# Performance work log

Hardware: AMD Instinct MI355X
Metric: run time of the kernel (lower is better)

## Reference

```python
import jax, jax.numpy as jnp
import numpy as np
from jax import lax

B, CIN, IMG, K = 128, 3, 112, 7
C = 1024      # hidden_channels * channel_dilation
HID = 512     # hidden_channels
HW = (IMG // K) ** 2  # 256 patches
EPS = 1e-5


def _prelu(x, a):
    return jnp.where(x > 0, x, a * x)


def _bn(x, g, b):
    # BatchNorm2d with track_running_stats=False: always uses batch stats
    m = x.mean(axis=(0, 2, 3), keepdims=True)
    v = x.var(axis=(0, 2, 3), keepdims=True)
    return (x - m) * lax.rsqrt(v + EPS) * g[None, :, None, None] + b[None, :, None, None]


def setup_inputs() -> dict:
    key = jax.random.key(0)
    ks = jax.random.split(key, 16)
    d = {
        'x':  jax.random.normal(ks[0], (B, CIN, IMG, IMG), jnp.float32),
        'w0': jax.random.normal(ks[1], (C, CIN, K, K), jnp.float32) * 0.05,
        'b0': jax.random.normal(ks[2], (C,), jnp.float32) * 0.01,
        'a0': jnp.full((1,), 0.25, jnp.float32),
    }
    for i in range(1, 4):
        kw, kb = jax.random.split(jax.random.fold_in(key, i))
        d[f'w{i}'] = jax.random.normal(kw, (C, C), jnp.float32) * 0.02
        d[f'b{i}'] = jax.random.normal(kb, (C,), jnp.float32) * 0.01
        d[f'g{i}'] = jnp.ones((C,), jnp.float32)
        d[f'bt{i}'] = jnp.zeros((C,), jnp.float32)
        d[f'p{i}'] = jnp.full((1,), 0.25, jnp.float32)
    d['pos'] = jax.random.normal(ks[3], (1, HW, C), jnp.float32)
    d['am'] = jnp.full((1,), 0.25, jnp.float32)
    d['wm'] = jax.random.normal(ks[4], (HID, C), jnp.float32) * 0.03
    d['bm'] = jax.random.normal(ks[5], (HID,), jnp.float32) * 0.01
    pkeys = jax.random.split(ks[6], B)
    d['perm'] = jax.vmap(lambda k: jax.random.permutation(k, HW))(pkeys).astype(jnp.int32)
    return d


def reference(x, w0, b0, a0,
              w1, b1, g1, bt1, p1,
              w2, b2, g2, bt2, p2,
              w3, b3, g3, bt3, p3,
              pos, am, wm, bm, perm):
    # patch-embed conv: stride = kernel_size -> [B, C, 16, 16]
    h = lax.conv_general_dilated(x, w0, (K, K), 'VALID',
                                 dimension_numbers=('NCHW', 'OIHW', 'NCHW'))
    h = _prelu(h + b0[None, :, None, None], a0)
    for w, b, g, bt, p in ((w1, b1, g1, bt1, p1),
                           (w2, b2, g2, bt2, p2),
                           (w3, b3, g3, bt3, p3)):
        h = jnp.einsum('bchw,dc->bdhw', h, w) + b[None, :, None, None]  # 1x1 conv
        h = _prelu(_bn(h, g, bt), p)
    Bn, Cn, Hn, Wn = h.shape
    enc = h.reshape(Bn, Cn, Hn * Wn).transpose(0, 2, 1)  # [B, HW, C]
    enc = enc + pos                                      # private: add pos embedding
    enc = _prelu(enc, am) @ wm.T + bm                    # mixer -> [B, HW, HID]
    # private: per-sample token permutation (single batched gather)
    return jnp.take_along_axis(enc, perm[:, :, None], axis=1)
```

## Files before the change

kernel.cpp:

```cpp
#include <hip/hip_runtime.h>
#include <hip/hip_bf16.h>
#include <stdint.h>


typedef __attribute__((ext_vector_type(8))) short bf16x8;
typedef __attribute__((ext_vector_type(4))) float f32x4;

__device__ __forceinline__ float bf2f(uint32_t u) {
  union { uint32_t i; float f; } v; v.i = u << 16; return v.f;
}
__device__ __forceinline__ ushort f2bf(float f) {
  union { float f; uint32_t i; } v; v.f = f;
  uint32_t i = v.i;
  return (ushort)((i + 0x7FFFu + ((i >> 16) & 1u)) >> 16);
}

template<int EPI, int XB>
__global__ void __launch_bounds__(512, 2)
gemm_kernel(const ushort* __restrict__ A, const ushort* __restrict__ Bw,
            const float* __restrict__ bias, const float* __restrict__ alpha,
            void* __restrict__ outp, float* __restrict__ part,
            const int* __restrict__ inv, int K, int Dout)
{
  __shared__ __align__(16) ushort At[2][256 * 64];
  __shared__ __align__(16) ushort Bt[2][256 * 64];
  const int tid  = threadIdx.x;
  const int lane = tid & 63;
  const int wid  = tid >> 6;
  const int wm   = wid >> 2;
  const int wn   = wid & 3;

  const int s = blockIdx.x;
  const int j = s >> 3;
  const int x = j & ((1 << XB) - 1);
  const int y = ((j >> XB) << 3) | (s & 7);
  const int t0 = y << 8;
  const int d0 = x << 8;

  f32x4 acc[8][4] = {};

  const int lrow8 = lane >> 3;
  const int csrc  = (lane & 7) ^ lrow8;
  const int NT = K >> 6;

  auto stage = [&](int t, int buf) {
    const int k0 = t << 6;
#pragma unroll
    for (int g = 0; g < 4; ++g) {
      int rb = (g << 6) + (wid << 3);
      const ushort* ga = A + (size_t)(t0 + rb + lrow8) * K + k0 + (csrc << 3);
      __builtin_amdgcn_global_load_lds(
          (const __attribute__((address_space(1))) uint32_t*)ga,
          (__attribute__((address_space(3))) uint32_t*)(&At[buf][rb << 6]), 16, 0, 0);
      const ushort* gb = Bw + (size_t)(d0 + rb + lrow8) * K + k0 + (csrc << 3);
      __builtin_amdgcn_global_load_lds(
          (const __attribute__((address_space(1))) uint32_t*)gb,
          (__attribute__((address_space(3))) uint32_t*)(&Bt[buf][rb << 6]), 16, 0, 0);
    }
  };

  stage(0, 0);
  stage(1, 1);

  for (int t = 0; t < NT; ++t) {
    const int cur = t & 1;
    if (t + 1 < NT) { asm volatile("s_waitcnt vmcnt(8)" ::: "memory"); }
    else            { asm volatile("s_waitcnt vmcnt(0)" ::: "memory"); }
    __builtin_amdgcn_s_barrier();

    __builtin_amdgcn_s_setprio(1);
#pragma unroll
    for (int kk = 0; kk < 2; ++kk) {
      const int kc = (kk << 2) + (lane >> 4);
      bf16x8 af[8], bfr[4];
#pragma unroll
      for (int m = 0; m < 8; ++m) {
        int row = (wm << 7) + (m << 4) + (lane & 15);
        af[m] = *(const bf16x8*)&At[cur][(row << 6) + ((kc ^ (row & 7)) << 3)];
      }
#pragma unroll
      for (int n = 0; n < 4; ++n) {
        int col = (wn << 6) + (n << 4) + (lane & 15);
        bfr[n] = *(const bf16x8*)&Bt[cur][(col << 6) + ((kc ^ (col & 7)) << 3)];
      }
#pragma unroll
      for (int m = 0; m < 8; ++m)
#pragma unroll
        for (int n = 0; n < 4; ++n)
          acc[m][n] = __builtin_amdgcn_mfma_f32_16x16x32_bf16(af[m], bfr[n], acc[m][n], 0, 0, 0);
    }
    __builtin_amdgcn_s_setprio(0);
    asm volatile("s_waitcnt lgkmcnt(0)" ::: "memory");
    __builtin_amdgcn_s_barrier();
    asm volatile("" ::: "memory");
    if (t + 2 < NT) stage(t + 2, cur);
  }

  float a0v = (EPI == 0) ? alpha[0] : 0.0f;
  float sA[4], s2A[4];
#pragma unroll
  for (int n = 0; n < 4; ++n) { sA[n] = 0.f; s2A[n] = 0.f; }

#pragma unroll
  for (int n = 0; n < 4; ++n) {
    int d = d0 + (wn << 6) + (n << 4) + (lane & 15);
    float bs = bias[d];
#pragma unroll
    for (int m = 0; m < 8; ++m) {
      int tb = t0 + (wm << 7) + (m << 4) + ((lane >> 4) << 2);
#pragma unroll
      for (int r = 0; r < 4; ++r) {
        float v = acc[m][n][r] + bs;
        if (EPI == 0) v = v > 0.f ? v : a0v * v;
        if (EPI == 1) { sA[n] += v; s2A[n] += v * v; }
        if (EPI == 2) {
          int row = tb + r;
          int orow = (row & ~255) | inv[row];
          ((float*)outp)[(size_t)orow * Dout + d] = v;
        } else {
          ((ushort*)outp)[(size_t)(tb + r) * Dout + d] = f2bf(v);
        }
      }
    }
  }

  if (EPI == 1) {
    float2* sm = (float2*)&At[0][0];
    int slot = (wm << 2) | (lane >> 4);
#pragma unroll
    for (int n = 0; n < 4; ++n) {
      int c = (wn << 6) + (n << 4) + (lane & 15);
      sm[slot * 256 + c] = make_float2(sA[n], s2A[n]);
    }
    __syncthreads();
    if (tid < 256) {
      float ss = 0.f, ss2 = 0.f;
      for (int q = 0; q < 8; ++q) {
        float2 v = sm[q * 256 + tid];
        ss += v.x; ss2 += v.y;
      }
      part[(size_t)y * 2048 + d0 + tid]        = ss;
      part[(size_t)y * 2048 + 1024 + d0 + tid] = ss2;
    }
  }
}

__global__ void bnfold_kernel(const float* __restrict__ part, const float* __restrict__ g,
                              const float* __restrict__ bt, float* __restrict__ scsh) {
  int d = (blockIdx.x << 8) + threadIdx.x;
  float s = 0.f, s2 = 0.f;
  for (int j = 0; j < 128; ++j) { s += part[j * 2048 + d]; s2 += part[j * 2048 + 1024 + d]; }
  float mean = s * (1.f / 32768.f);
  float var  = s2 * (1.f / 32768.f) - mean * mean;
  float sc = g[d] * rsqrtf(var + 1e-5f);
  scsh[d] = sc;
  scsh[1024 + d] = bt[d] - mean * sc;
}

template<bool MIX>
__global__ void bnact_kernel(ushort* __restrict__ Y, const float* __restrict__ scsh,
                             const float* __restrict__ p, const float* __restrict__ pos,
                             const float* __restrict__ am) {
  size_t i = (((size_t)blockIdx.x << 8) + threadIdx.x) << 3;
  int d = (int)(i & 1023);
  float pp = p[0];
  float aa = MIX ? am[0] : 0.f;
  float pv[8];
  if (MIX) {
    int prow = (int)((i >> 10) & 255);
    const float4* pb = (const float4*)(pos + ((size_t)prow << 10) + d);
    float4 pA = pb[0], pB = pb[1];
    pv[0]=pA.x; pv[1]=pA.y; pv[2]=pA.z; pv[3]=pA.w;
    pv[4]=pB.x; pv[5]=pB.y; pv[6]=pB.z; pv[7]=pB.w;
  }
  uint4 raw = *(const uint4*)(Y + i);
  uint32_t w[4] = {raw.x, raw.y, raw.z, raw.w};
  uint32_t o[4];
#pragma unroll
  for (int q = 0; q < 4; ++q) {
    int dd = d + q * 2;
    float v0 = bf2f(w[q] & 0xFFFFu) * scsh[dd]     + scsh[1024 + dd];
    float v1 = bf2f(w[q] >> 16)     * scsh[dd + 1] + scsh[1024 + dd + 1];
    v0 = v0 > 0.f ? v0 : pp * v0;
    v1 = v1 > 0.f ? v1 : pp * v1;
    if (MIX) {
      v0 += pv[2 * q];     v1 += pv[2 * q + 1];
      v0 = v0 > 0.f ? v0 : aa * v0;
      v1 = v1 > 0.f ? v1 : aa * v1;
    }
    o[q] = (uint32_t)f2bf(v0) | ((uint32_t)f2bf(v1) << 16);
  }
  *(uint4*)(Y + i) = make_uint4(o[0], o[1], o[2], o[3]);
}

__global__ void invperm_kernel(const int* __restrict__ perm, int* __restrict__ inv) {
  int t = (blockIdx.x << 8) + threadIdx.x;
  inv[(t & ~255) + perm[t]] = t & 255;
}

__global__ void f2b_kernel(const float* __restrict__ in, ushort* __restrict__ out, int n) {
  int i = (blockIdx.x << 8) + threadIdx.x;
  if (i < n) out[i] = f2bf(in[i]);
}

__global__ void padw0_kernel(const float* __restrict__ w0, ushort* __restrict__ o) {
  int d = blockIdx.x, j = threadIdx.x;
  o[d * 256 + j] = (j < 147) ? f2bf(w0[d * 147 + j]) : (ushort)0;
}

__global__ void im2col_kernel(const float* __restrict__ x, ushort* __restrict__ P) {
  int t = blockIdx.x;
  int j = threadIdx.x;
  ushort v = 0;
  if (j < 147) {
    int b = t >> 8, pidx = t & 255;
    int pi = pidx >> 4, pj = pidx & 15;
    int cin = j / 49, rem = j - cin * 49;
    int dy = rem / 7, dx = rem - dy * 7;
    v = f2bf(x[(size_t)(b * 3 + cin) * 12544 + (size_t)(pi * 7 + dy) * 112 + (pj * 7 + dx)]);
  }
  P[(size_t)t * 256 + j] = v;
}

extern "C" void kernel_launch(void* const* d_in, const int* in_sizes, int n_in,
                              void* d_out, int out_size, void* d_ws, size_t ws_size,
                              hipStream_t stream) {
  const float* x   = (const float*)d_in[0];
  const float* w0  = (const float*)d_in[1];
  const float* b0  = (const float*)d_in[2];
  const float* a0  = (const float*)d_in[3];
  const float* w1  = (const float*)d_in[4];
  const float* b1  = (const float*)d_in[5];
  const float* g1  = (const float*)d_in[6];
  const float* bt1 = (const float*)d_in[7];
  const float* p1  = (const float*)d_in[8];
  const float* w2  = (const float*)d_in[9];
  const float* b2  = (const float*)d_in[10];
  const float* g2  = (const float*)d_in[11];
  const float* bt2 = (const float*)d_in[12];
  const float* p2  = (const float*)d_in[13];
  const float* w3  = (const float*)d_in[14];
  const float* b3  = (const float*)d_in[15];
  const float* g3  = (const float*)d_in[16];
  const float* bt3 = (const float*)d_in[17];
  const float* p3  = (const float*)d_in[18];
  const float* pos = (const float*)d_in[19];
  const float* am  = (const float*)d_in[20];
  const float* wm  = (const float*)d_in[21];
  const float* bm  = (const float*)d_in[22];
  const int*  perm = (const int*)d_in[23];

  char* ws = (char*)d_ws;
  ushort* B0   = (ushort*)ws;
  ushort* B1   = (ushort*)(ws + 67108864);
  float*  part = (float*)(ws + 134217728);
  float*  scsh = (float*)(ws + 134217728 + 2097152);
  int*    inv  = (int*)  (ws + 134217728 + 2097152 + 8192);
  ushort* wbuf = (ushort*)(ws + 134217728 + 2097152 + 8192 + 131072);

  invperm_kernel<<<dim3(128), dim3(256), 0, stream>>>(perm, inv);
  im2col_kernel<<<dim3(32768), dim3(256), 0, stream>>>(x, B1);
  padw0_kernel<<<dim3(1024), dim3(256), 0, stream>>>(w0, wbuf);

  gemm_kernel<0, 2><<<dim3(512), dim3(512), 0, stream>>>(
      B1, wbuf, b0, a0, (void*)B0, nullptr, nullptr, 256, 1024);

  f2b_kernel<<<dim3(4096), dim3(256), 0, stream>>>(w1, wbuf, 1048576);
  gemm_kernel<1, 2><<<dim3(512), dim3(512), 0, stream>>>(
      B0, wbuf, b1, nullptr, (void*)B1, part, nullptr, 1024, 1024);
  bnfold_kernel<<<dim3(4), dim3(256), 0, stream>>>(part, g1, bt1, scsh);
  bnact_kernel<false><<<dim3(16384), dim3(256), 0, stream>>>(B1, scsh, p1, nullptr, nullptr);

  f2b_kernel<<<dim3(4096), dim3(256), 0, stream>>>(w2, wbuf, 1048576);
  gemm_kernel<1, 2><<<dim3(512), dim3(512), 0, stream>>>(
      B1, wbuf, b2, nullptr, (void*)B0, part, nullptr, 1024, 1024);
  bnfold_kernel<<<dim3(4), dim3(256), 0, stream>>>(part, g2, bt2, scsh);
  bnact_kernel<false><<<dim3(16384), dim3(256), 0, stream>>>(B0, scsh, p2, nullptr, nullptr);

  f2b_kernel<<<dim3(4096), dim3(256), 0, stream>>>(w3, wbuf, 1048576);
  gemm_kernel<1, 2><<<dim3(512), dim3(512), 0, stream>>>(
      B0, wbuf, b3, nullptr, (void*)B1, part, nullptr, 1024, 1024);
  bnfold_kernel<<<dim3(4), dim3(256), 0, stream>>>(part, g3, bt3, scsh);
  bnact_kernel<true><<<dim3(16384), dim3(256), 0, stream>>>(B1, scsh, p3, pos, am);

  f2b_kernel<<<dim3(2048), dim3(256), 0, stream>>>(wm, wbuf, 524288);
  gemm_kernel<2, 1><<<dim3(256), dim3(512), 0, stream>>>(
      B1, wbuf, bm, nullptr, d_out, nullptr, inv, 1024, 512);
}
```

Measured before the change: 468.4 us.

## Interleave LDS reads, global prefetch and MFMA in barrier-separated phases

Restructures the GEMM main loop into four phases per k-tile. Each phase reads a quarter of the A/B fragments from LDS, issues part of the next tile's global-to-LDS loads, and runs 16 MFMAs between barriers, in the style of a ping-pong schedule. A is now prefetched one tile ahead and B two tiles ahead, so memory traffic spreads across the compute. The epilogue hoists the bias loads and computes the gather index once per row. The extra barriers add sync overhead and risk stalls if the waitcnt accounting is off.

Result: faster. 418.4 us (-10.7%).

```diff
diff --git a/kernel.cpp b/kernel.cpp
--- a/kernel.cpp
+++ b/kernel.cpp
@@ -43,83 +43,116 @@
   const int csrc  = (lane & 7) ^ lrow8;
   const int NT = K >> 6;
 
-  auto stage = [&](int t, int buf) {
+  auto stageA = [&](int t, int buf, int h) {
     const int k0 = t << 6;
 #pragma unroll
-    for (int g = 0; g < 4; ++g) {
-      int rb = (g << 6) + (wid << 3);
-      const ushort* ga = A + (size_t)(t0 + rb + lrow8) * K + k0 + (csrc << 3);
+    for (int i = 0; i < 2; ++i) {
+      int rb = (h << 7) + (wid << 4) + (i << 3);
+      const ushort* gp = A + (size_t)(t0 + rb + lrow8) * K + k0 + (csrc << 3);
       __builtin_amdgcn_global_load_lds(
-          (const __attribute__((address_space(1))) uint32_t*)ga,
+          (const __attribute__((address_space(1))) uint32_t*)gp,
           (__attribute__((address_space(3))) uint32_t*)(&At[buf][rb << 6]), 16, 0, 0);
-      const ushort* gb = Bw + (size_t)(d0 + rb + lrow8) * K + k0 + (csrc << 3);
+    }
+  };
+  auto stageB = [&](int t, int buf, int h) {
+    const int k0 = t << 6;
+#pragma unroll
+    for (int i = 0; i < 2; ++i) {
+      int rb = (h << 7) + (wid << 4) + (i << 3);
+      const ushort* gp = Bw + (size_t)(d0 + rb + lrow8) * K + k0 + (csrc << 3);
       __builtin_amdgcn_global_load_lds(
-          (const __attribute__((address_space(1))) uint32_t*)gb,
+          (const __attribute__((address_space(1))) uint32_t*)gp,
           (__attribute__((address_space(3))) uint32_t*)(&Bt[buf][rb << 6]), 16, 0, 0);
     }
   };
-
-  stage(0, 0);
-  stage(1, 1);
+  auto readA = [&](bf16x8* af, int buf, int mh, int kk) {
+    const int kc = (kk << 2) + (lane >> 4);
+#pragma unroll
+    for (int m = 0; m < 4; ++m) {
+      int row = (wm << 7) + (mh << 6) + (m << 4) + (lane & 15);
+      af[m] = *(const bf16x8*)&At[buf][(row << 6) + ((kc ^ (row & 7)) << 3)];
+    }
+  };
+  auto readB = [&](bf16x8* bf, int buf, int kk) {
+    const int kc = (kk << 2) + (lane >> 4);
+#pragma unroll
+    for (int n = 0; n < 4; ++n) {
+      int col = (wn << 6) + (n << 4) + (lane & 15);
+      bf[n] = *(const bf16x8*)&Bt[buf][(col << 6) + ((kc ^ (col & 7)) << 3)];
+    }
+  };
+  auto mfma16 = [&](const bf16x8* af, const bf16x8* bf, int mh) {
+    __builtin_amdgcn_s_setprio(1);
+#pragma unroll
+    for (int m = 0; m < 4; ++m)
+#pragma unroll
+      for (int n = 0; n < 4; ++n)
+        acc[(mh << 2) + m][n] =
+            __builtin_amdgcn_mfma_f32_16x16x32_bf16(af[m], bf[n], acc[(mh << 2) + m][n], 0, 0, 0);
+    __builtin_amdgcn_s_setprio(0);
+  };
+
+  stageA(0, 0, 0); stageA(0, 0, 1);
+  stageB(0, 0, 0); stageB(0, 0, 1);
+  if (NT > 1) { stageB(1, 1, 0); stageB(1, 1, 1); }
+  if (NT > 1) { asm volatile("s_waitcnt vmcnt(4)" ::: "memory"); }
+  else        { asm volatile("s_waitcnt vmcnt(0)" ::: "memory"); }
+  __builtin_amdgcn_s_barrier();
+
+  bf16x8 af[4], bfA[4], bfB[4];
 
   for (int t = 0; t < NT; ++t) {
     const int cur = t & 1;
-    if (t + 1 < NT) { asm volatile("s_waitcnt vmcnt(8)" ::: "memory"); }
-    else            { asm volatile("s_waitcnt vmcnt(0)" ::: "memory"); }
-    __builtin_amdgcn_s_barrier();
-
-    __builtin_amdgcn_s_setprio(1);
-#pragma unroll
-    for (int kk = 0; kk < 2; ++kk) {
-      const int kc = (kk << 2) + (lane >> 4);
-      bf16x8 af[8], bfr[4];
-#pragma unroll
-      for (int m = 0; m < 8; ++m) {
-        int row = (wm << 7) + (m << 4) + (lane & 15);
-        af[m] = *(const bf16x8*)&At[cur][(row << 6) + ((kc ^ (row & 7)) << 3)];
-      }
+    const bool haveN1 = (t + 1 < NT), haveN2 = (t + 2 < NT);
+
+    readA(af, cur, 0, 0);
+    readB(bfA, cur, 0);
+    if (haveN1) stageA(t + 1, cur ^ 1, 0);
+    __builtin_amdgcn_s_barrier();
+    mfma16(af, bfA, 0);
+    __builtin_amdgcn_s_barrier();
+
+    readA(af, cur, 1, 0);
+    if (haveN1) stageA(t + 1, cur ^ 1, 1);
+    __builtin_amdgcn_s_barrier();
+    mfma16(af, bfA, 1);
+    __builtin_amdgcn_s_barrier();
+
+    readA(af, cur, 0, 1);
+    readB(bfB, cur, 1);
+    __builtin_amdgcn_s_barrier();
+    mfma16(af, bfB, 0);
+    __builtin_amdgcn_s_barrier();
+
+    readA(af, cur, 1, 1);
+    if (haveN2) { stageB(t + 2, cur, 0); stageB(t + 2, cur, 1); }
+    if (haveN2)      { asm volatile("s_waitcnt vmcnt(4)" ::: "memory"); }
+    else if (haveN1) { asm volatile("s_waitcnt vmcnt(0)" ::: "memory"); }
+    __builtin_amdgcn_s_barrier();
+    mfma16(af, bfB, 1);
+    __builtin_amdgcn_s_barrier();
+  }
+
+  float bs[4];
+#pragma unroll
+  for (int n = 0; n < 4; ++n) bs[n] = bias[d0 + (wn << 6) + (n << 4) + (lane & 15)];
+  float a0v = (EPI == 0) ? alpha[0] : 0.0f;
+  float sA[4] = {0.f, 0.f, 0.f, 0.f}, s2A[4] = {0.f, 0.f, 0.f, 0.f};
+
+#pragma unroll
+  for (int m = 0; m < 8; ++m) {
+#pragma unroll
+    for (int r = 0; r < 4; ++r) {
+      int row = t0 + (wm << 7) + (m << 4) + ((lane >> 4) << 2) + r;
+      int orow = (EPI == 2) ? ((row & ~255) | inv[row]) : row;
 #pragma unroll
       for (int n = 0; n < 4; ++n) {
-        int col = (wn << 6) + (n << 4) + (lane & 15);
-        bfr[n] = *(const bf16x8*)&Bt[cur][(col << 6) + ((kc ^ (col & 7)) << 3)];
-      }
-#pragma unroll
-      for (int m = 0; m < 8; ++m)
-#pragma unroll
-        for (int n = 0; n < 4; ++n)
-          acc[m][n] = __builtin_amdgcn_mfma_f32_16x16x32_bf16(af[m], bfr[n], acc[m][n], 0, 0, 0);
-    }
-    __builtin_amdgcn_s_setprio(0);
-    asm volatile("s_waitcnt lgkmcnt(0)" ::: "memory");
-    __builtin_amdgcn_s_barrier();
-    asm volatile("" ::: "memory");
-    if (t + 2 < NT) stage(t + 2, cur);
-  }
-
-  float a0v = (EPI == 0) ? alpha[0] : 0.0f;
-  float sA[4], s2A[4];
-#pragma unroll
-  for (int n = 0; n < 4; ++n) { sA[n] = 0.f; s2A[n] = 0.f; }
-
-#pragma unroll
-  for (int n = 0; n < 4; ++n) {
-    int d = d0 + (wn << 6) + (n << 4) + (lane & 15);
-    float bs = bias[d];
-#pragma unroll
-    for (int m = 0; m < 8; ++m) {
-      int tb = t0 + (wm << 7) + (m << 4) + ((lane >> 4) << 2);
-#pragma unroll
-      for (int r = 0; r < 4; ++r) {
-        float v = acc[m][n][r] + bs;
+        int d = d0 + (wn << 6) + (n << 4) + (lane & 15);
+        float v = acc[m][n][r] + bs[n];
         if (EPI == 0) v = v > 0.f ? v : a0v * v;
         if (EPI == 1) { sA[n] += v; s2A[n] += v * v; }
-        if (EPI == 2) {
-          int row = tb + r;
-          int orow = (row & ~255) | inv[row];
-          ((float*)outp)[(size_t)orow * Dout + d] = v;
-        } else {
-          ((ushort*)outp)[(size_t)(tb + r) * Dout + d] = f2bf(v);
-        }
+        if (EPI == 2) ((float*)outp)[(size_t)orow * Dout + d] = v;
+        else          ((ushort*)outp)[(size_t)row * Dout + d] = f2bf(v);
       }
     }
   }
@@ -127,6 +160,7 @@
   if (EPI == 1) {
     float2* sm = (float2*)&At[0][0];
     int slot = (wm << 2) | (lane >> 4);
+    __syncthreads();
 #pragma unroll
     for (int n = 0; n < 4; ++n) {
       int c = (wn << 6) + (n << 4) + (lane & 15);
```

## Restructure GEMM main loop into interleaved half-tile loads and MFMA phases

Applied to the files above, without the earlier changes.

Rewrites the GEMM K-loop as four sub-phases per tile. Each phase issues LDS reads for half the A rows, launches the global-to-LDS copies for the next A tile and for B two tiles ahead, and runs 16 MFMAs between barriers. It also makes K and Dout template constants, precomputes the swizzled LDS addresses, and reorders the epilogue so the inverse-permutation index is loaded once per row. The aim is finer overlap of memory traffic with MFMA work and less address arithmetic, at the cost of many more barriers per tile and a subtler buffer-reuse pattern.

Measured after the change: 405.0 us. 13.5% less time.

```diff
diff --git a/kernel.cpp b/kernel.cpp
--- a/kernel.cpp
+++ b/kernel.cpp
@@ -15,12 +15,12 @@
   return (ushort)((i + 0x7FFFu + ((i >> 16) & 1u)) >> 16);
 }
 
-template<int EPI, int XB>
+template<int EPI, int XB, int K, int DOUT>
 __global__ void __launch_bounds__(512, 2)
 gemm_kernel(const ushort* __restrict__ A, const ushort* __restrict__ Bw,
             const float* __restrict__ bias, const float* __restrict__ alpha,
             void* __restrict__ outp, float* __restrict__ part,
-            const int* __restrict__ inv, int K, int Dout)
+            const int* __restrict__ inv)
 {
   __shared__ __align__(16) ushort At[2][256 * 64];
   __shared__ __align__(16) ushort Bt[2][256 * 64];
@@ -39,87 +39,123 @@
 
   f32x4 acc[8][4] = {};
 
+  const int swz = (((lane >> 4) ^ (lane & 7)) << 4);
+  const char* LA0 = (const char*)&At[0][0] + ((((wm << 7) + (lane & 15))) << 7) + swz;
+  const char* LA1 = (const char*)&At[0][0] + ((((wm << 7) + (lane & 15))) << 7) + (swz ^ 64);
+  const char* LB0 = (const char*)&Bt[0][0] + ((((wn << 6) + (lane & 15))) << 7) + swz;
+  const char* LB1 = (const char*)&Bt[0][0] + ((((wn << 6) + (lane & 15))) << 7) + (swz ^ 64);
+
   const int lrow8 = lane >> 3;
   const int csrc  = (lane & 7) ^ lrow8;
-  const int NT = K >> 6;
-
-  auto stage = [&](int t, int buf) {
-    const int k0 = t << 6;
-#pragma unroll
-    for (int g = 0; g < 4; ++g) {
-      int rb = (g << 6) + (wid << 3);
-      const ushort* ga = A + (size_t)(t0 + rb + lrow8) * K + k0 + (csrc << 3);
-      __builtin_amdgcn_global_load_lds(
-          (const __attribute__((address_space(1))) uint32_t*)ga,
-          (__attribute__((address_space(3))) uint32_t*)(&At[buf][rb << 6]), 16, 0, 0);
-      const ushort* gb = Bw + (size_t)(d0 + rb + lrow8) * K + k0 + (csrc << 3);
-      __builtin_amdgcn_global_load_lds(
-          (const __attribute__((address_space(1))) uint32_t*)gb,
-          (__attribute__((address_space(3))) uint32_t*)(&Bt[buf][rb << 6]), 16, 0, 0);
-    }
-  };
-
-  stage(0, 0);
-  stage(1, 1);
-
-  for (int t = 0; t < NT; ++t) {
-    const int cur = t & 1;
-    if (t + 1 < NT) { asm volatile("s_waitcnt vmcnt(8)" ::: "memory"); }
-    else            { asm volatile("s_waitcnt vmcnt(0)" ::: "memory"); }
-    __builtin_amdgcn_s_barrier();
-
-    __builtin_amdgcn_s_setprio(1);
-#pragma unroll
-    for (int kk = 0; kk < 2; ++kk) {
-      const int kc = (kk << 2) + (lane >> 4);
-      bf16x8 af[8], bfr[4];
-#pragma unroll
-      for (int m = 0; m < 8; ++m) {
-        int row = (wm << 7) + (m << 4) + (lane & 15);
-        af[m] = *(const bf16x8*)&At[cur][(row << 6) + ((kc ^ (row & 7)) << 3)];
-      }
+  const ushort* gAw = A  + (size_t)(t0 + (wid << 4) + lrow8) * K + (csrc << 3);
+  const ushort* gBw = Bw + (size_t)(d0 + (wid << 4) + lrow8) * K + (csrc << 3);
+  char* stA = (char*)&At[0][0] + (wid << 11);
+  char* stB = (char*)&Bt[0][0] + (wid << 11);
+
+#define STAGE_A(T, BUF, H) do {                                                          \
+    __builtin_amdgcn_global_load_lds(                                                    \
+      (const __attribute__((address_space(1))) uint32_t*)(gAw + (size_t)((H)*128)*K + ((size_t)(T) << 6)),     \
+      (__attribute__((address_space(3))) uint32_t*)(stA + (BUF)*32768 + (H)*16384), 16, 0, 0);                  \
+    __builtin_amdgcn_global_load_lds(                                                    \
+      (const __attribute__((address_space(1))) uint32_t*)(gAw + (size_t)((H)*128+8)*K + ((size_t)(T) << 6)),   \
+      (__attribute__((address_space(3))) uint32_t*)(stA + (BUF)*32768 + (H)*16384 + 1024), 16, 0, 0);           \
+  } while (0)
+#define STAGE_B(T, BUF, H) do {                                                          \
+    __builtin_amdgcn_global_load_lds(                                                    \
+      (const __attribute__((address_space(1))) uint32_t*)(gBw + (size_t)((H)*128)*K + ((size_t)(T) << 6)),     \
+      (__attribute__((address_space(3))) uint32_t*)(stB + (BUF)*32768 + (H)*16384), 16, 0, 0);                  \
+    __builtin_amdgcn_global_load_lds(                                                    \
+      (const __attribute__((address_space(1))) uint32_t*)(gBw + (size_t)((H)*128+8)*K + ((size_t)(T) << 6)),   \
+      (__attribute__((address_space(3))) uint32_t*)(stB + (BUF)*32768 + (H)*16384 + 1024), 16, 0, 0);           \
+  } while (0)
+
+#define RD_A(dst, BASE, CUR, MH) do {                                                    \
+    dst[0] = *(const bf16x8*)((BASE) + (CUR)*32768 + (MH)*8192 + 0);                     \
+    dst[1] = *(const bf16x8*)((BASE) + (CUR)*32768 + (MH)*8192 + 2048);                  \
+    dst[2] = *(const bf16x8*)((BASE) + (CUR)*32768 + (MH)*8192 + 4096);                  \
+    dst[3] = *(const bf16x8*)((BASE) + (CUR)*32768 + (MH)*8192 + 6144);                  \
+  } while (0)
+#define RD_B(dst, BASE, CUR) do {                                                        \
+    dst[0] = *(const bf16x8*)((BASE) + (CUR)*32768 + 0);                                 \
+    dst[1] = *(const bf16x8*)((BASE) + (CUR)*32768 + 2048);                              \
+    dst[2] = *(const bf16x8*)((BASE) + (CUR)*32768 + 4096);                              \
+    dst[3] = *(const bf16x8*)((BASE) + (CUR)*32768 + 6144);                              \
+  } while (0)
+#define MFMA16(AF, BF, MH) do {                                                          \
+    __builtin_amdgcn_s_setprio(1);                                                       \
+    _Pragma("unroll")                                                                    \
+    for (int m_ = 0; m_ < 4; ++m_)                                                       \
+      _Pragma("unroll")                                                                  \
+      for (int n_ = 0; n_ < 4; ++n_)                                                     \
+        acc[((MH) << 2) + m_][n_] = __builtin_amdgcn_mfma_f32_16x16x32_bf16(             \
+            AF[m_], BF[n_], acc[((MH) << 2) + m_][n_], 0, 0, 0);                         \
+    __builtin_amdgcn_s_setprio(0);                                                       \
+  } while (0)
+
+#define TILE_BODY(T, CUR, HN1, HN2) do {                                                 \
+    bf16x8 af[4], bfA[4], bfB[4];                                                        \
+                                                                                \
+    RD_A(af, LA0, CUR, 0); RD_B(bfA, LB0, CUR);                                          \
+    if (HN1) STAGE_A((T) + 1, (CUR) ^ 1, 0);                                             \
+    __builtin_amdgcn_s_barrier();                                                        \
+    MFMA16(af, bfA, 0);                                                                  \
+    __builtin_amdgcn_s_barrier();                                                        \
+                                                                                \
+    RD_A(af, LA0, CUR, 1);                                                               \
+    if (HN1) STAGE_A((T) + 1, (CUR) ^ 1, 1);                                             \
+    __builtin_amdgcn_s_barrier();                                                        \
+    MFMA16(af, bfA, 1);                                                                  \
+    __builtin_amdgcn_s_barrier();                                                        \
+                                                                                \
+    RD_A(af, LA1, CUR, 0); RD_B(bfB, LB1, CUR);                                          \
+    __builtin_amdgcn_s_barrier();                                                        \
+    MFMA16(af, bfB, 0);                                                                  \
+    __builtin_amdgcn_s_barrier();                                                        \
+                                                                                \
+    RD_A(af, LA1, CUR, 1);                                                               \
+    if (HN2) { STAGE_B((T) + 2, CUR, 0); STAGE_B((T) + 2, CUR, 1); }                     \
+    if (HN2)      { asm volatile("s_waitcnt vmcnt(4)" ::: "memory"); }                   \
+    else if (HN1) { asm volatile("s_waitcnt vmcnt(0)" ::: "memory"); }                   \
+    __builtin_amdgcn_s_barrier();                                                        \
+    MFMA16(af, bfB, 1);                                                                  \
+    __builtin_amdgcn_s_barrier();                                                        \
+  } while (0)
+
+  constexpr int NT = K >> 6;
+
+  STAGE_A(0, 0, 0); STAGE_A(0, 0, 1);
+  STAGE_B(0, 0, 0); STAGE_B(0, 0, 1);
+  STAGE_B(1, 1, 0); STAGE_B(1, 1, 1);
+  asm volatile("s_waitcnt vmcnt(4)" ::: "memory");
+  __builtin_amdgcn_s_barrier();
+
+#pragma unroll 1
+  for (int tp = 0; tp < NT; tp += 2) {
+    const bool more = (tp + 2 < NT);
+    TILE_BODY(tp,     0, true, more);
+    TILE_BODY(tp + 1, 1, more, more);
+  }
+
+  float bs[4];
+#pragma unroll
+  for (int n = 0; n < 4; ++n) bs[n] = bias[d0 + (wn << 6) + (n << 4) + (lane & 15)];
+  float a0v = (EPI == 0) ? alpha[0] : 0.0f;
+  float sA[4] = {0.f, 0.f, 0.f, 0.f}, s2A[4] = {0.f, 0.f, 0.f, 0.f};
+
+#pragma unroll
+  for (int m = 0; m < 8; ++m) {
+#pragma unroll
+    for (int r = 0; r < 4; ++r) {
+      int row = t0 + (wm << 7) + (m << 4) + ((lane >> 4) << 2) + r;
+      int orow = (EPI == 2) ? ((row & ~255) | inv[row]) : row;
 #pragma unroll
       for (int n = 0; n < 4; ++n) {
-        int col = (wn << 6) + (n << 4) + (lane & 15);
-        bfr[n] = *(const bf16x8*)&Bt[cur][(col << 6) + ((kc ^ (col & 7)) << 3)];
-      }
-#pragma unroll
-      for (int m = 0; m < 8; ++m)
-#pragma unroll
-        for (int n = 0; n < 4; ++n)
-          acc[m][n] = __builtin_amdgcn_mfma_f32_16x16x32_bf16(af[m], bfr[n], acc[m][n], 0, 0, 0);
-    }
-    __builtin_amdgcn_s_setprio(0);
-    asm volatile("s_waitcnt lgkmcnt(0)" ::: "memory");
-    __builtin_amdgcn_s_barrier();
-    asm volatile("" ::: "memory");
-    if (t + 2 < NT) stage(t + 2, cur);
-  }
-
-  float a0v = (EPI == 0) ? alpha[0] : 0.0f;
-  float sA[4], s2A[4];
-#pragma unroll
-  for (int n = 0; n < 4; ++n) { sA[n] = 0.f; s2A[n] = 0.f; }
-
-#pragma unroll
-  for (int n = 0; n < 4; ++n) {
-    int d = d0 + (wn << 6) + (n << 4) + (lane & 15);
-    float bs = bias[d];
-#pragma unroll
-    for (int m = 0; m < 8; ++m) {
-      int tb = t0 + (wm << 7) + (m << 4) + ((lane >> 4) << 2);
-#pragma unroll
-      for (int r = 0; r < 4; ++r) {
-        float v = acc[m][n][r] + bs;
+        int d = d0 + (wn << 6) + (n << 4) + (lane & 15);
+        float v = acc[m][n][r] + bs[n];
         if (EPI == 0) v = v > 0.f ? v : a0v * v;
         if (EPI == 1) { sA[n] += v; s2A[n] += v * v; }
-        if (EPI == 2) {
-          int row = tb + r;
-          int orow = (row & ~255) | inv[row];
-          ((float*)outp)[(size_t)orow * Dout + d] = v;
-        } else {
-          ((ushort*)outp)[(size_t)(tb + r) * Dout + d] = f2bf(v);
-        }
+        if (EPI == 2) ((float*)outp)[(size_t)orow * DOUT + d] = v;
+        else          ((ushort*)outp)[(size_t)row * DOUT + d] = f2bf(v);
       }
     }
   }
@@ -127,6 +163,7 @@
   if (EPI == 1) {
     float2* sm = (float2*)&At[0][0];
     int slot = (wm << 2) | (lane >> 4);
+    __syncthreads();
 #pragma unroll
     for (int n = 0; n < 4; ++n) {
       int c = (wn << 6) + (n << 4) + (lane & 15);
@@ -143,6 +180,12 @@
       part[(size_t)y * 2048 + 1024 + d0 + tid] = ss2;
     }
   }
+#undef STAGE_A
+#undef STAGE_B
+#undef RD_A
+#undef RD_B
+#undef MFMA16
+#undef TILE_BODY
 }
 
 __global__ void bnfold_kernel(const float* __restrict__ part, const float* __restrict__ g,
@@ -262,28 +305,28 @@
   im2col_kernel<<<dim3(32768), dim3(256), 0, stream>>>(x, B1);
   padw0_kernel<<<dim3(1024), dim3(256), 0, stream>>>(w0, wbuf);
 
-  gemm_kernel<0, 2><<<dim3(512), dim3(512), 0, stream>>>(
-      B1, wbuf, b0, a0, (void*)B0, nullptr, nullptr, 256, 1024);
+  gemm_kernel<0, 2, 256, 1024><<<dim3(512), dim3(512), 0, stream>>>(
+      B1, wbuf, b0, a0, (void*)B0, nullptr, nullptr);
 
   f2b_kernel<<<dim3(4096), dim3(256), 0, stream>>>(w1, wbuf, 1048576);
-  gemm_kernel<1, 2><<<dim3(512), dim3(512), 0, stream>>>(
-      B0, wbuf, b1, nullptr, (void*)B1, part, nullptr, 1024, 1024);
+  gemm_kernel<1, 2, 1024, 1024><<<dim3(512), dim3(512), 0, stream>>>(
+      B0, wbuf, b1, nullptr, (void*)B1, part, nullptr);
   bnfold_kernel<<<dim3(4), dim3(256), 0, stream>>>(part, g1, bt1, scsh);
   bnact_kernel<false><<<dim3(16384), dim3(256), 0, stream>>>(B1, scsh, p1, nullptr, nullptr);
 
   f2b_kernel<<<dim3(4096), dim3(256), 0, stream>>>(w2, wbuf, 1048576);
-  gemm_kernel<1, 2><<<dim3(512), dim3(512), 0, stream>>>(
-      B1, wbuf, b2, nullptr, (void*)B0, part, nullptr, 1024, 1024);
+  gemm_kernel<1, 2, 1024, 1024><<<dim3(512), dim3(512), 0, stream>>>(
+      B1, wbuf, b2, nullptr, (void*)B0, part, nullptr);
   bnfold_kernel<<<dim3(4), dim3(256), 0, stream>>>(part, g2, bt2, scsh);
   bnact_kernel<false><<<dim3(16384), dim3(256), 0, stream>>>(B0, scsh, p2, nullptr, nullptr);
 
   f2b_kernel<<<dim3(4096), dim3(256), 0, stream>>>(w3, wbuf, 1048576);
-  gemm_kernel<1, 2><<<dim3(512), dim3(512), 0, stream>>>(
-      B0, wbuf, b3, nullptr, (void*)B1, part, nullptr, 1024, 1024);
+  gemm_kernel<1, 2, 1024, 1024><<<dim3(512), dim3(512), 0, stream>>>(
+      B0, wbuf, b3, nullptr, (void*)B1, part, nullptr);
   bnfold_kernel<<<dim3(4), dim3(256), 0, stream>>>(part, g3, bt3, scsh);
   bnact_kernel<true><<<dim3(16384), dim3(256), 0, stream>>>(B1, scsh, p3, pos, am);
 
   f2b_kernel<<<dim3(2048), dim3(256), 0, stream>>>(wm, wbuf, 524288);
-  gemm_kernel<2, 1><<<dim3(256), dim3(512), 0, stream>>>(
-      B1, wbuf, bm, nullptr, d_out, nullptr, inv, 1024, 512);
-}
+  gemm_kernel<2, 1, 1024, 512><<<dim3(256), dim3(512), 0, stream>>>(
+      B1, wbuf, bm, nullptr, d_out, nullptr, inv);
+}
```
